# Performance work log

Hardware: AMD Instinct MI355X
Metric: run time of the kernel (lower is better)

Reference implementation:

```python
import jax, jax.numpy as jnp
import numpy as np

NUM_ITERATIONS = 3


def squash(s):
    # s: [..., out_channels]; norm over last axis (matches torch squash on squeezed tensor)
    norm = jnp.linalg.norm(s, axis=-1, keepdims=True)
    return (norm ** 2 / (1.0 + norm ** 2)) * (s / norm)


def setup_inputs() -> dict:
    key = jax.random.key(0)
    k1, k2 = jax.random.split(key)
    B, R, C, O, I = 256, 192, 96, 16, 20
    x = jax.random.normal(k1, (B, R, I), dtype=jnp.float32)
    W = jax.random.normal(k2, (R, C, O, I), dtype=jnp.float32)
    return {"x": x, "W": W}


def reference(x, W):
    # u_hat[b,r,c,o] = W[r,c,o,i] @ x[b,r,i]  (torch: matmul(W, x[i]) per batch element)
    u_hat = jnp.einsum('rcoi,bri->brco', W, x)  # [B,R,C,O]
    R, C = W.shape[0], W.shape[1]
    b_ij = jnp.zeros((R, C), dtype=x.dtype)  # shared across batch (torch b_ij is [1,R,C,1])
    v_j = None
    for it in range(NUM_ITERATIONS):
        c_ij = jax.nn.softmax(b_ij, axis=0)                 # softmax over routes (dim=1 in torch)
        s_j = jnp.einsum('rc,brco->bco', c_ij, u_hat)        # weighted sum over routes
        v_j = squash(s_j)                                    # [B,C,O]
        if it < NUM_ITERATIONS - 1:
            # agreement: <u_hat, v_j> averaged over batch (torch mean(dim=0))
            a_ij = jnp.einsum('brco,bco->rc', u_hat, v_j) / x.shape[0]
            b_ij = b_ij + a_ij
    return v_j  # [B, num_capsules, out_channels] (torch returns trailing singleton [B,C,O,1])
```

## Files before the change

### kernel.cpp

```cpp
#include <hip/hip_runtime.h>


#define R_ 192
#define C_ 96
#define O_ 16
#define I_ 20
#define B_ 256
#define K1 3840
#define N_ 1536
#define NKT 30

typedef unsigned short u16;
typedef __attribute__((ext_vector_type(8))) short short8;
typedef __attribute__((ext_vector_type(4))) float floatx4;

__device__ inline float bf2f(u16 h) {
  union { unsigned int u; float f; } x; x.u = ((unsigned int)h) << 16; return x.f;
}
__device__ inline u16 f2bf(float f) {
  union { float f; unsigned int u; } x; x.f = f;
  unsigned int r = x.u + 0x7FFFu + ((x.u >> 16) & 1u);
  return (u16)(r >> 16);
}
__device__ inline unsigned int pack2(float a, float b) {
  return (unsigned int)f2bf(a) | ((unsigned int)f2bf(b) << 16);
}
__device__ inline void async16(const u16* g, u16* l) {
  __builtin_amdgcn_global_load_lds(
      (__attribute__((address_space(1))) void*)(unsigned long long)g,
      (__attribute__((address_space(3))) void*)(unsigned int)(unsigned long long)l,
      16, 0, 0);
}

__global__ void k_prep(const float* __restrict__ W, const float* __restrict__ X,
                       u16* __restrict__ WtT, u16* __restrict__ Xk,
                       u16* __restrict__ xT, float* __restrict__ bij) {
  int bid = blockIdx.x;
  if (bid < 5760) {
    int t = (bid * 256 + threadIdx.x) << 2;
    int n = t / K1, k = t - n * K1;
    int c = n >> 4, o = n & 15;
    const float* Wn = W + (size_t)(c * O_ + o) * I_;
    u16 h[4];
    #pragma unroll
    for (int e = 0; e < 4; ++e) {
      int ke = k + e, r = ke / I_, i = ke - r * I_;
      h[e] = f2bf(Wn[(size_t)r * (C_ * O_ * I_) + i]);
    }
    ushort4 o4; o4.x = h[0]; o4.y = h[1]; o4.z = h[2]; o4.w = h[3];
    *(ushort4*)&WtT[t] = o4;
  } else if (bid < 6000) {
    __shared__ u16 tile[64][72];
    int idx = bid - 5760;
    int kb = (idx % 60) << 6, bb = (idx / 60) << 6;
    int brow = threadIdx.x >> 4;
    int kq = (threadIdx.x & 15) << 2;
    #pragma unroll
    for (int p = 0; p < 4; ++p) {
      int bl = p * 16 + brow;
      float4 v = *(const float4*)(X + (size_t)(bb + bl) * K1 + kb + kq);
      ushort4 h;
      h.x = f2bf(v.x); h.y = f2bf(v.y); h.z = f2bf(v.z); h.w = f2bf(v.w);
      *(ushort4*)(Xk + (size_t)(bb + bl) * K1 + kb + kq) = h;
      tile[kq + 0][bl] = h.x;
      tile[kq + 1][bl] = h.y;
      tile[kq + 2][bl] = h.z;
      tile[kq + 3][bl] = h.w;
    }
    __syncthreads();
    int kr = threadIdx.x >> 3;
    int bq = (threadIdx.x & 7) << 3;
    #pragma unroll
    for (int q = 0; q < 2; ++q) {
      int kl = q * 32 + kr;
      *(uint4*)(xT + (size_t)(kb + kl) * B_ + bb + bq) = *(const uint4*)&tile[kl][bq];
    }
  } else {
    int t = ((bid - 6000) * 256 + threadIdx.x) << 2;
    if (t < R_ * C_) *(float4*)&bij[t] = (float4){0.f, 0.f, 0.f, 0.f};
  }
}

__device__ inline uint4 scale_b8(uint4 raw, int kg, const float* smrow) {
  int r0 = kg / I_;
  int bnd = (r0 + 1) * I_ - kg;
  float s0 = smrow[r0];
  float s1 = smrow[(r0 + 1 < R_) ? r0 + 1 : R_ - 1];
  union { uint4 q; u16 h[8]; } u; u.q = raw;
  #pragma unroll
  for (int j = 0; j < 8; ++j)
    u.h[j] = f2bf(bf2f(u.h[j]) * ((j < bnd) ? s0 : s1));
  return u.q;
}

__global__ __launch_bounds__(256) void gemm1(
    const u16* __restrict__ A, const u16* __restrict__ Bt,
    const float* __restrict__ bij, int doScale,
    float* __restrict__ out, u16* __restrict__ vT,
    float preScale, int last) {
  __shared__ u16 As[2][4][1024];
  __shared__ u16 Bs[2][4][1024];
  __shared__ float sm[2][192];
  int tid = threadIdx.x;
  int w = tid >> 6, lane = tid & 63;
  if (doScale && w < 2) {
    int c = ((int)blockIdx.x << 1) + w;
    float e0 = bij[c * R_ + lane];
    float e1 = bij[c * R_ + lane + 64];
    float e2 = bij[c * R_ + lane + 128];
    float mx = fmaxf(e0, fmaxf(e1, e2));
    #pragma unroll
    for (int off = 32; off > 0; off >>= 1) mx = fmaxf(mx, __shfl_xor(mx, off));
    e0 = expf(e0 - mx); e1 = expf(e1 - mx); e2 = expf(e2 - mx);
    float s = e0 + e1 + e2;
    #pragma unroll
    for (int off = 32; off > 0; off >>= 1) s += __shfl_xor(s, off);
    float inv = 1.0f / s;
    sm[w][lane] = e0 * inv;
    sm[w][lane + 64] = e1 * inv;
    sm[w][lane + 128] = e2 * inv;
  }

  long n0 = (long)blockIdx.x * 32, m0 = (long)blockIdx.y * 32;
  const u16* Ab = A + m0 * K1;
  const u16* Bb = Bt + n0 * K1;
  int srow = ((w & 1) << 4) + (lane >> 2);
  int scol = (lane & 3) << 3;
  int subA = w >> 1;
  int rb = (w & 1) << 9;
  const u16* Ag = Ab + (long)srow * K1 + subA * 32 + scol;
  const u16* Bg = Bb + (long)srow * K1 + subA * 32 + scol;
  int rowb = tid >> 3;
  int kc = (tid & 7) << 3;
  const u16* Bgs = Bb + (long)rowb * K1 + kc;
  const float* smrow = &sm[rowb >> 4][0];
  int wm = (w >> 1) << 4, wn = (w & 1) << 4;
  int quad = lane >> 4, lrow = lane & 15;
  floatx4 acc = (floatx4){0.f, 0.f, 0.f, 0.f};

  async16(Ag, &As[0][subA][rb]);
  async16(Ag + 64, &As[0][subA + 2][rb]);
  uint4 pb0, pb1;
  if (doScale) {
    pb0 = *(const uint4*)Bgs;
    pb1 = *(const uint4*)(Bgs + 64);
  } else {
    async16(Bg, &Bs[0][subA][rb]);
    async16(Bg + 64, &Bs[0][subA + 2][rb]);
  }
  __syncthreads();

  int p = 0;
  for (int kt = 0; kt < NKT; ++kt) {
    if (doScale) {
      int kg = (kt << 7) + kc;
      int sub = kc >> 5;
      *(uint4*)&Bs[p][sub][rowb * 32 + (kc & 31)] = scale_b8(pb0, kg, smrow);
      *(uint4*)&Bs[p][sub + 2][rowb * 32 + (kc & 31)] = scale_b8(pb1, kg + 64, smrow);
      __syncthreads();
    } else if (kt > 0) {
      __syncthreads();
    }
    if (kt + 1 < NKT) {
      int kk = (kt + 1) << 7;
      async16(Ag + kk, &As[p ^ 1][subA][rb]);
      async16(Ag + kk + 64, &As[p ^ 1][subA + 2][rb]);
      if (doScale) {
        pb0 = *(const uint4*)(Bgs + kk);
        pb1 = *(const uint4*)(Bgs + kk + 64);
      } else {
        async16(Bg + kk, &Bs[p ^ 1][subA][rb]);
        async16(Bg + kk + 64, &Bs[p ^ 1][subA + 2][rb]);
      }
    }
    #pragma unroll
    for (int s = 0; s < 4; ++s) {
      short8 af = *(const short8*)&As[p][s][(wm + lrow) * 32 + (quad << 3)];
      short8 bfr = *(const short8*)&Bs[p][s][(wn + lrow) * 32 + (quad << 3)];
      acc = __builtin_amdgcn_mfma_f32_16x16x32_bf16(af, bfr, acc, 0, 0, 0);
    }
    p ^= 1;
  }

  float v0 = acc[0] * preScale, v1 = acc[1] * preScale;
  float v2 = acc[2] * preScale, v3 = acc[3] * preScale;
  float q0 = v0 * v0, q1 = v1 * v1, q2 = v2 * v2, q3 = v3 * v3;
  #pragma unroll
  for (int off = 1; off < 16; off <<= 1) {
    q0 += __shfl_xor(q0, off);
    q1 += __shfl_xor(q1, off);
    q2 += __shfl_xor(q2, off);
    q3 += __shfl_xor(q3, off);
  }
  v0 *= q0 / ((1.0f + q0) * sqrtf(q0));
  v1 *= q1 / ((1.0f + q1) * sqrtf(q1));
  v2 *= q2 / ((1.0f + q2) * sqrtf(q2));
  v3 *= q3 / ((1.0f + q3) * sqrtf(q3));
  int n = (int)n0 + wn + lrow;
  int b = (int)m0 + wm + (quad << 2);
  if (last) {
    out[(size_t)(b + 0) * N_ + n] = v0;
    out[(size_t)(b + 1) * N_ + n] = v1;
    out[(size_t)(b + 2) * N_ + n] = v2;
    out[(size_t)(b + 3) * N_ + n] = v3;
  } else {
    uint2 pk;
    pk.x = pack2(v0, v1);
    pk.y = pack2(v2, v3);
    *(uint2*)&vT[(size_t)n * B_ + b] = pk;
  }
}

__global__ __launch_bounds__(256) void gemm2_agree(
    const u16* __restrict__ A, const u16* __restrict__ Bt,
    const u16* __restrict__ WtT, float* __restrict__ bij) {
  const int K = 256;
  __shared__ u16 As[2][2][128 * 32];
  __shared__ u16 Bs[2][2][64 * 32];
  int tid = threadIdx.x;
  long m0 = (long)blockIdx.x * 128, n0 = (long)blockIdx.y * 64;
  const u16* Ab = A + m0 * K;
  const u16* Bb = Bt + n0 * K;
  int srow = tid >> 2;
  int scol = (tid & 3) << 3;
  int w = tid >> 6, lane = tid & 63;
  int wm = (w >> 1) << 6, wn = (w & 1) << 5;
  int quad = lane >> 4, lrow = lane & 15;
  int wb = w << 9;
  const u16* Ag0 = Ab + (long)srow * K + scol;
  const u16* Ag1 = Ab + (long)(srow + 64) * K + scol;
  const u16* Bg0 = Bb + (long)srow * K + scol;
  floatx4 acc[4][2];
  #pragma unroll
  for (int a = 0; a < 4; ++a)
    #pragma unroll
    for (int b = 0; b < 2; ++b) acc[a][b] = (floatx4){0.f, 0.f, 0.f, 0.f};

  async16(Ag0, &As[0][0][wb]);
  async16(Ag1, &As[0][0][2048 + wb]);
  async16(Ag0 + 32, &As[0][1][wb]);
  async16(Ag1 + 32, &As[0][1][2048 + wb]);
  async16(Bg0, &Bs[0][0][wb]);
  async16(Bg0 + 32, &Bs[0][1][wb]);

  int p = 0;
  #pragma unroll
  for (int kt = 0; kt < 4; ++kt) {
    __syncthreads();
    if (kt + 1 < 4) {
      int kk = (kt + 1) << 6;
      async16(Ag0 + kk, &As[p ^ 1][0][wb]);
      async16(Ag1 + kk, &As[p ^ 1][0][2048 + wb]);
      async16(Ag0 + kk + 32, &As[p ^ 1][1][wb]);
      async16(Ag1 + kk + 32, &As[p ^ 1][1][2048 + wb]);
      async16(Bg0 + kk, &Bs[p ^ 1][0][wb]);
      async16(Bg0 + kk + 32, &Bs[p ^ 1][1][wb]);
    }
    #pragma unroll
    for (int s = 0; s < 2; ++s) {
      short8 af[4], bfr[2];
      #pragma unroll
      for (int ms = 0; ms < 4; ++ms)
        af[ms] = *(const short8*)&As[p][s][(wm + ms * 16 + lrow) * 32 + (quad << 3)];
      #pragma unroll
      for (int ns = 0; ns < 2; ++ns)
        bfr[ns] = *(const short8*)&Bs[p][s][(wn + ns * 16 + lrow) * 32 + (quad << 3)];
      #pragma unroll
      for (int ms = 0; ms < 4; ++ms)
        #pragma unroll
        for (int ns = 0; ns < 2; ++ns)
          acc[ms][ns] = __builtin_amdgcn_mfma_f32_16x16x32_bf16(
              af[ms], bfr[ns], acc[ms][ns], 0, 0, 0);
    }
    p ^= 1;
  }
  #pragma unroll
  for (int ms = 0; ms < 4; ++ms) {
    int rowbase = (int)m0 + wm + ms * 16;
    int r_lo = rowbase / I_;
    int r_hi = (rowbase + 15) / I_;
    int bnd = (r_lo + 1) * I_;
    int rowl = rowbase + (quad << 2);
    #pragma unroll
    for (int ns = 0; ns < 2; ++ns) {
      int col = (int)n0 + wn + ns * 16 + lrow;
      uint2 wv = *(const uint2*)&WtT[(size_t)col * K1 + rowl];
      u16 h[4];
      h[0] = (u16)(wv.x & 0xffff); h[1] = (u16)(wv.x >> 16);
      h[2] = (u16)(wv.y & 0xffff); h[3] = (u16)(wv.y >> 16);
      float p0 = 0.f, p1 = 0.f;
      #pragma unroll
      for (int e = 0; e < 4; ++e) {
        float pr = acc[ms][ns][e] * bf2f(h[e]);
        if (rowl + e < bnd) p0 += pr; else p1 += pr;
      }
      #pragma unroll
      for (int off = 32; off > 0; off >>= 1) {
        p0 += __shfl_xor(p0, off);
        p1 += __shfl_xor(p1, off);
      }
      if (lane == 0) {
        int c = col >> 4;
        atomicAdd(&bij[c * R_ + r_lo], p0 * (1.0f / 256.0f));
        atomicAdd(&bij[c * R_ + r_hi], p1 * (1.0f / 256.0f));
      }
    }
  }
}

extern "C" void kernel_launch(void* const* d_in, const int* in_sizes, int n_in,
                              void* d_out, int out_size, void* d_ws, size_t ws_size,
                              hipStream_t stream) {
  const float* X = (const float*)d_in[0];
  const float* W = (const float*)d_in[1];
  float* out = (float*)d_out;
  char* ws = (char*)d_ws;
  u16*  WtT = (u16*)(ws);
  u16*  Xk  = (u16*)(ws + 11796480);
  u16*  xT  = (u16*)(ws + 13762560);
  u16*  vT  = (u16*)(ws + 15728640);
  float* bij = (float*)(ws + 16515072);

  k_prep<<<6018, 256, 0, stream>>>(W, X, WtT, Xk, xT, bij);

  for (int it = 0; it < 3; ++it) {
    gemm1<<<dim3(48, 8), 256, 0, stream>>>(
        Xk, WtT, bij, it > 0, out, vT,
        it == 0 ? (1.0f / 192.0f) : 1.0f, it == 2 ? 1 : 0);
    if (it < 2)
      gemm2_agree<<<dim3(30, 24), 256, 0, stream>>>(xT, vT, WtT, bij);
  }
}
```

Before: 173.6 us.

## Triple-buffer gemm1 K-loop with explicit vmcnt waits and reorganized LDS layout

Moves the gemm1 main loop from double to triple buffering of the A and B tiles, prefetching two K-tiles ahead with async loads. Completion is tracked with manual s_waitcnt vmcnt and raw s_barrier instead of __syncthreads. The LDS layout changes so each wave's loads and MFMA fragment reads use flat contiguous offsets, and all fragments are loaded before the MFMAs. The aim is to hide global-load latency better, at the cost of more LDS and registers and hand-tuned wait counts that must match the number of outstanding loads.

```diff
diff --git a/kernel.cpp b/kernel.cpp
--- a/kernel.cpp
+++ b/kernel.cpp
@@ -93,13 +93,13 @@
   return u.q;
 }
 
-__global__ __launch_bounds__(256) void gemm1(
+__global__ __launch_bounds__(256, 3) void gemm1(
     const u16* __restrict__ A, const u16* __restrict__ Bt,
     const float* __restrict__ bij, int doScale,
     float* __restrict__ out, u16* __restrict__ vT,
     float preScale, int last) {
-  __shared__ u16 As[2][4][1024];
-  __shared__ u16 Bs[2][4][1024];
+  __shared__ u16 As[3][4096];
+  __shared__ u16 Bs[3][4096];
   __shared__ float sm[2][192];
   int tid = threadIdx.x;
   int w = tid >> 6, lane = tid & 63;
@@ -124,63 +124,93 @@
   long n0 = (long)blockIdx.x * 32, m0 = (long)blockIdx.y * 32;
   const u16* Ab = A + m0 * K1;
   const u16* Bb = Bt + n0 * K1;
-  int srow = ((w & 1) << 4) + (lane >> 2);
-  int scol = (lane & 3) << 3;
-  int subA = w >> 1;
-  int rb = (w & 1) << 9;
-  const u16* Ag = Ab + (long)srow * K1 + subA * 32 + scol;
-  const u16* Bg = Bb + (long)srow * K1 + subA * 32 + scol;
-  int rowb = tid >> 3;
-  int kc = (tid & 7) << 3;
-  const u16* Bgs = Bb + (long)rowb * K1 + kc;
+  int l31 = lane & 31;
+  int aS = w >> 1;
+  int aK = ((w << 1) + (lane >> 5)) & 3;
+  const u16* AgA = Ab + (long)l31 * K1 + aS * 32 + aK * 8;
+  const u16* BgA = Bb + (long)l31 * K1 + aS * 32 + aK * 8;
+  int ldsLo = w << 9;
+  int ldsHi = 2048 + (w << 9);
+  int rowb = tid & 31;
+  int kq = tid >> 5;
+  const u16* Bgs = Bb + (long)rowb * K1 + kq * 8;
+  int wA0 = ((((kq) >> 2) << 7) + (((kq) & 3) << 5) + rowb) << 3;
+  int wA1 = ((((kq + 8) >> 2) << 7) + (((kq + 8) & 3) << 5) + rowb) << 3;
   const float* smrow = &sm[rowb >> 4][0];
+  int kgB0 = kq << 3, kgB1 = (kq + 8) << 3;
   int wm = (w >> 1) << 4, wn = (w & 1) << 4;
   int quad = lane >> 4, lrow = lane & 15;
+  int rdA = (quad << 8) + ((wm + lrow) << 3);
+  int rdB = (quad << 8) + ((wn + lrow) << 3);
   floatx4 acc = (floatx4){0.f, 0.f, 0.f, 0.f};
-
-  async16(Ag, &As[0][subA][rb]);
-  async16(Ag + 64, &As[0][subA + 2][rb]);
-  uint4 pb0, pb1;
+  uint4 pb00, pb01, pb10, pb11, pb20, pb21;
+
+  async16(AgA, &As[0][ldsLo]);
+  async16(AgA + 64, &As[0][ldsHi]);
+  async16(AgA + 128, &As[1][ldsLo]);
+  async16(AgA + 192, &As[1][ldsHi]);
+  async16(AgA + 256, &As[2][ldsLo]);
+  async16(AgA + 320, &As[2][ldsHi]);
   if (doScale) {
-    pb0 = *(const uint4*)Bgs;
-    pb1 = *(const uint4*)(Bgs + 64);
+    pb00 = *(const uint4*)(Bgs);       pb01 = *(const uint4*)(Bgs + 64);
+    pb10 = *(const uint4*)(Bgs + 128); pb11 = *(const uint4*)(Bgs + 192);
+    pb20 = *(const uint4*)(Bgs + 256); pb21 = *(const uint4*)(Bgs + 320);
   } else {
-    async16(Bg, &Bs[0][subA][rb]);
-    async16(Bg + 64, &Bs[0][subA + 2][rb]);
+    async16(BgA, &Bs[0][ldsLo]);       async16(BgA + 64, &Bs[0][ldsHi]);
+    async16(BgA + 128, &Bs[1][ldsLo]); async16(BgA + 192, &Bs[1][ldsHi]);
+    async16(BgA + 256, &Bs[2][ldsLo]); async16(BgA + 320, &Bs[2][ldsHi]);
   }
   __syncthreads();
 
-  int p = 0;
-  for (int kt = 0; kt < NKT; ++kt) {
-    if (doScale) {
-      int kg = (kt << 7) + kc;
-      int sub = kc >> 5;
-      *(uint4*)&Bs[p][sub][rowb * 32 + (kc & 31)] = scale_b8(pb0, kg, smrow);
-      *(uint4*)&Bs[p][sub + 2][rowb * 32 + (kc & 31)] = scale_b8(pb1, kg + 64, smrow);
-      __syncthreads();
-    } else if (kt > 0) {
-      __syncthreads();
-    }
-    if (kt + 1 < NKT) {
-      int kk = (kt + 1) << 7;
-      async16(Ag + kk, &As[p ^ 1][subA][rb]);
-      async16(Ag + kk + 64, &As[p ^ 1][subA + 2][rb]);
-      if (doScale) {
-        pb0 = *(const uint4*)(Bgs + kk);
-        pb1 = *(const uint4*)(Bgs + kk + 64);
-      } else {
-        async16(Bg + kk, &Bs[p ^ 1][subA][rb]);
-        async16(Bg + kk + 64, &Bs[p ^ 1][subA + 2][rb]);
-      }
-    }
-    #pragma unroll
-    for (int s = 0; s < 4; ++s) {
-      short8 af = *(const short8*)&As[p][s][(wm + lrow) * 32 + (quad << 3)];
-      short8 bfr = *(const short8*)&Bs[p][s][(wn + lrow) * 32 + (quad << 3)];
-      acc = __builtin_amdgcn_mfma_f32_16x16x32_bf16(af, bfr, acc, 0, 0, 0);
-    }
-    p ^= 1;
-  }
+#define G1_STEP(BUF, PB0, PB1, VM, DOPF)                                   \
+  {                                                                        \
+    asm volatile("s_waitcnt vmcnt(" #VM ")" ::: "memory");                 \
+    if (doScale) {                                                         \
+      *(uint4*)&Bs[BUF][wA0] = scale_b8(PB0, kOff + kgB0, smrow);          \
+      *(uint4*)&Bs[BUF][wA1] = scale_b8(PB1, kOff + kgB1, smrow);          \
+      asm volatile("s_waitcnt lgkmcnt(0)" ::: "memory");                   \
+    }                                                                      \
+    __builtin_amdgcn_s_barrier();                                          \
+    short8 af0 = *(const short8*)&As[BUF][rdA];                            \
+    short8 af1 = *(const short8*)&As[BUF][rdA + 1024];                     \
+    short8 af2 = *(const short8*)&As[BUF][rdA + 2048];                     \
+    short8 af3 = *(const short8*)&As[BUF][rdA + 3072];                     \
+    short8 bf0 = *(const short8*)&Bs[BUF][rdB];                            \
+    short8 bf1 = *(const short8*)&Bs[BUF][rdB + 1024];                     \
+    short8 bf2 = *(const short8*)&Bs[BUF][rdB + 2048];                     \
+    short8 bf3 = *(const short8*)&Bs[BUF][rdB + 3072];                     \
+    asm volatile("s_waitcnt lgkmcnt(0)" ::: "memory");                     \
+    __builtin_amdgcn_sched_barrier(0);                                     \
+    __builtin_amdgcn_s_barrier();                                          \
+    if (DOPF) {                                                            \
+      async16(AgA + kOff + 384, &As[BUF][ldsLo]);                          \
+      async16(AgA + kOff + 448, &As[BUF][ldsHi]);                          \
+      if (doScale) {                                                       \
+        PB0 = *(const uint4*)(Bgs + kOff + 384);                           \
+        PB1 = *(const uint4*)(Bgs + kOff + 448);                           \
+      } else {                                                             \
+        async16(BgA + kOff + 384, &Bs[BUF][ldsLo]);                        \
+        async16(BgA + kOff + 448, &Bs[BUF][ldsHi]);                        \
+      }                                                                    \
+    }                                                                      \
+    acc = __builtin_amdgcn_mfma_f32_16x16x32_bf16(af0, bf0, acc, 0, 0, 0); \
+    acc = __builtin_amdgcn_mfma_f32_16x16x32_bf16(af1, bf1, acc, 0, 0, 0); \
+    acc = __builtin_amdgcn_mfma_f32_16x16x32_bf16(af2, bf2, acc, 0, 0, 0); \
+    acc = __builtin_amdgcn_mfma_f32_16x16x32_bf16(af3, bf3, acc, 0, 0, 0); \
+    kOff += 128;                                                           \
+  }
+
+  int kOff = 0;
+  #pragma unroll 1
+  for (int c3 = 0; c3 < 9; ++c3) {
+    G1_STEP(0, pb00, pb01, 8, 1)
+    G1_STEP(1, pb10, pb11, 8, 1)
+    G1_STEP(2, pb20, pb21, 8, 1)
+  }
+  G1_STEP(0, pb00, pb01, 8, 0)
+  G1_STEP(1, pb10, pb11, 4, 0)
+  G1_STEP(2, pb20, pb21, 0, 0)
+#undef G1_STEP
 
   float v0 = acc[0] * preScale, v1 = acc[1] * preScale;
   float v2 = acc[2] * preScale, v3 = acc[3] * preScale;
```

Result: slower. 206.8 us (+19.2%).
